# Optimization experiments

Hardware: AMD Instinct MI355X
Metric: run time of the kernel (lower is better)

Reference implementation:

```python
import jax, jax.numpy as jnp
import numpy as np

N = 50000   # nodes
E = 800000  # edges
F_IN, F_HID, F_OUT = 128, 96, 40


def setup_inputs() -> dict:
    key = jax.random.key(0)
    ks = jax.random.split(key, 9)
    x = jax.random.normal(ks[0], (N, F_IN), dtype=jnp.float32)
    edge_index = jax.random.randint(ks[1], (2, E), 0, N, dtype=jnp.int32)
    def lin(k, fi, fo):
        s = 1.0 / np.sqrt(fi)
        return jax.random.uniform(k, (fi, fo), jnp.float32, -s, s)
    W1 = lin(ks[2], F_IN, F_HID)
    b1 = jnp.zeros((F_HID,), jnp.float32)
    W2 = lin(ks[3], F_HID, F_HID)
    b2 = jnp.zeros((F_HID,), jnp.float32)
    Wout = lin(ks[4], F_HID, F_OUT)
    bout = jnp.zeros((F_OUT,), jnp.float32)
    return {"x": x, "edge_index": edge_index, "W1": W1, "b1": b1,
            "W2": W2, "b2": b2, "Wout": Wout, "bout": bout}


def _gcn_norm(edge_index, n):
    # add self-loops, symmetric degree normalization (PyG GCNConv default)
    loops = jnp.arange(n, dtype=edge_index.dtype)
    src = jnp.concatenate([edge_index[0], loops])
    dst = jnp.concatenate([edge_index[1], loops])
    deg = jax.ops.segment_sum(jnp.ones_like(dst, dtype=jnp.float32), dst,
                              num_segments=n)
    dinv = jnp.where(deg > 0, jax.lax.rsqrt(deg), 0.0)
    norm = dinv[src] * dinv[dst]   # [E+N]
    return src, dst, norm


def _gcn_layer(h, src, dst, norm, W, b, n):
    # linear transform, then normalized scatter-add aggregation, then bias
    h = h @ W                                 # [N, Fout]
    msg = h[src] * norm[:, None]              # gather + scale
    agg = jax.ops.segment_sum(msg, dst, num_segments=n)
    return agg + b


def reference(x, edge_index, W1, b1, W2, b2, Wout, bout):
    n = x.shape[0]
    src, dst, norm = _gcn_norm(edge_index, n)
    h = jax.nn.relu(_gcn_layer(x, src, dst, norm, W1, b1, n))
    h = jax.nn.relu(_gcn_layer(h, src, dst, norm, W2, b2, n))
    return h @ Wout + bout
```

## Files before the change

kernel.cpp:

```cpp
#include <hip/hip_runtime.h>
#include <hip/hip_fp16.h>

#define N_NODES 50000
#define N_EDGES 800000
#define F_INN   128
#define F_HID   96
#define F_OUTT  40
#define SLOTS   64

typedef _Float16 half8 __attribute__((ext_vector_type(8)));
typedef float    floatx4 __attribute__((ext_vector_type(4)));

template <int FI, typename TIN, bool SCALE>
__device__ __forceinline__ void mfma_gemm_body(
        const TIN* __restrict__ X, const __half* __restrict__ BTg,
        const float* __restrict__ dinv, float4* __restrict__ Th4, int n, int bx) {
    __shared__ __half BTl[96 * 136];
    __half* OUTl = BTl;
    int tid = threadIdx.x;
    {
        const int4* s = reinterpret_cast<const int4*>(BTg);
        int4* d = reinterpret_cast<int4*>(BTl);
        for (int i = tid; i < 96 * 136 / 8; i += 256) d[i] = s[i];
    }
    __syncthreads();

    int lane = tid & 63, w = tid >> 6;
    int lm = lane & 15, q = lane >> 4;
    int base = bx * 64 + w * 16;
    int node = base + lm;
    int nclamp = min(node, n - 1);
    const TIN* Xrow = X + (size_t)nclamp * FI;

    floatx4 cf[6];
    #pragma unroll
    for (int t = 0; t < 6; ++t) cf[t] = (floatx4){0.f, 0.f, 0.f, 0.f};

    constexpr int KS = FI / 32;
    #pragma unroll
    for (int ks = 0; ks < KS; ++ks) {
        half8 bv;
        if constexpr (sizeof(TIN) == 4) {
            const float4* xr = reinterpret_cast<const float4*>(Xrow + 32 * ks + q * 8);
            float4 f0 = xr[0], f1 = xr[1];
            union { half8 v; __half2 h[4]; } b;
            b.h[0] = __floats2half2_rn(f0.x, f0.y);
            b.h[1] = __floats2half2_rn(f0.z, f0.w);
            b.h[2] = __floats2half2_rn(f1.x, f1.y);
            b.h[3] = __floats2half2_rn(f1.z, f1.w);
            bv = b.v;
        } else {
            bv = *reinterpret_cast<const half8*>(Xrow + 32 * ks + q * 8);
        }
        #pragma unroll
        for (int t = 0; t < 6; ++t) {
            half8 a = *reinterpret_cast<const half8*>(
                &BTl[(t * 16 + lm) * 136 + q * 8 + 32 * ks]);
            cf[t] = __builtin_amdgcn_mfma_f32_16x16x32_f16(a, bv, cf[t], 0, 0, 0);
        }
    }

    float dv = 1.0f;
    if constexpr (SCALE) dv = dinv[nclamp];

    __syncthreads();

    __half* orow = OUTl + (w * 16 + lm) * 104;
    #pragma unroll
    for (int t = 0; t < 6; ++t) {
        union { int2 i2; __half2 h[2]; } u;
        u.h[0] = __floats2half2_rn(dv * cf[t][0], dv * cf[t][1]);
        u.h[1] = __floats2half2_rn(dv * cf[t][2], dv * cf[t][3]);
        *reinterpret_cast<int2*>(&orow[t * 16 + q * 4]) = u.i2;
    }
    #pragma unroll
    for (int R = 0; R < 3; ++R) {
        int nl = lane >> 2, c = (lane & 3) + 4 * R;
        float4 v = *reinterpret_cast<const float4*>(&OUTl[(w * 16 + nl) * 104 + c * 8]);
        int gn = base + nl;
        if (gn < n) Th4[(size_t)gn * 12 + c] = v;
    }
}

__global__ __launch_bounds__(256) void fill_gemm1_kernel(
        const int* __restrict__ src, const int* __restrict__ dst,
        int* __restrict__ cnt, int* __restrict__ csr_pad,
        int e, const float* __restrict__ X, const __half* __restrict__ BT1,
        float4* __restrict__ Th4, int n, int nFB) {
    if ((int)blockIdx.x < nFB) {
        int i = blockIdx.x * 512 + threadIdx.x;
        int j = i + 256;
        bool bi = i < e, bj = j < e;
        int di = 0, dj = 0, si, sj, pi, pj;
        if (bi) { di = dst[i]; si = src[i]; }
        if (bj) { dj = dst[j]; sj = src[j]; }
        if (bi) pi = atomicAdd(&cnt[di], 1);
        if (bj) pj = atomicAdd(&cnt[dj], 1);
        if (bi && pi < SLOTS) csr_pad[di * SLOTS + pi] = si;
        if (bj && pj < SLOTS) csr_pad[dj * SLOTS + pj] = sj;
    } else {
        mfma_gemm_body<F_INN, float, false>(X, BT1, nullptr, Th4, n, blockIdx.x - nFB);
    }
}

template <int FI, typename TIN, bool SCALE>
__global__ __launch_bounds__(256) void mfma_gemm_kernel(
        const TIN* __restrict__ X, const __half* __restrict__ BTg,
        const float* __restrict__ dinv, float4* __restrict__ Th4, int n) {
    mfma_gemm_body<FI, TIN, SCALE>(X, BTg, dinv, Th4, n, blockIdx.x);
}

__global__ void wt_kernel(const float* __restrict__ W1, const float* __restrict__ W2,
                          __half* __restrict__ BT1, __half* __restrict__ BT2) {
    int i = blockIdx.x * 256 + threadIdx.x;
    if (i < 96 * 128) {
        int j = i / 128, k = i - j * 128;
        BT1[j * 136 + k] = __float2half(W1[k * 96 + j]);
    } else if (i < 96 * 128 + 96 * 96) {
        int t = i - 96 * 128;
        int j = t / 96, k = t - j * 96;
        BT2[j * 136 + k] = __float2half(W2[k * 96 + j]);
    }
}

__global__ __launch_bounds__(256) void scale_dinv_kernel(
        const int* __restrict__ cnt, float* __restrict__ dinv,
        float4* __restrict__ Th4, int n) {
    int i = blockIdx.x * 256 + threadIdx.x;
    if (i < n) dinv[i] = rsqrtf((float)min(cnt[i], SLOTS) + 1.0f);
    if (i >= n * 12) return;
    int node = i / 12;
    float s = rsqrtf((float)min(cnt[node], SLOTS) + 1.0f);
    union { float4 f4; __half2 h[4]; } u;
    u.f4 = Th4[i];
    #pragma unroll
    for (int q = 0; q < 4; ++q) {
        float2 t = __half22float2(u.h[q]);
        u.h[q] = __floats2half2_rn(s * t.x, s * t.y);
    }
    Th4[i] = u.f4;
}

__global__ __launch_bounds__(256) void agg_kernel(
        const __half2* __restrict__ T, const int* __restrict__ cnt,
        const int* __restrict__ csr_pad, const float* __restrict__ dinv,
        const float* __restrict__ bias, __half2* __restrict__ H, int n) {
    int lane = threadIdx.x & 63;
    int node = __builtin_amdgcn_readfirstlane(blockIdx.x * 4 + (threadIdx.x >> 6));
    if (node >= n) return;
    int fl = min(lane, 47);

    float dn = dinv[node];
    float2 self = __half22float2(T[(size_t)node * 48 + fl]);
    float accx = self.x, accy = self.y;

    const int* row = csr_pad + (size_t)node * SLOTS;
    int deg = min(cnt[node], SLOTS);
    int idx = 0;
    for (; idx + 8 <= deg; idx += 8) {
        int s[8];
        #pragma unroll
        for (int u = 0; u < 8; ++u) s[u] = row[idx + u];
        float2 f[8];
        #pragma unroll
        for (int u = 0; u < 8; ++u) f[u] = __half22float2(T[(size_t)s[u] * 48 + fl]);
        #pragma unroll
        for (int u = 0; u < 8; ++u) {
            accx += f[u].x;
            accy += f[u].y;
        }
    }
    for (; idx < deg; ++idx) {
        int s = row[idx];
        float2 f = __half22float2(T[(size_t)s * 48 + fl]);
        accx += f.x;
        accy += f.y;
    }
    if (lane < 48) {
        float2 b = reinterpret_cast<const float2*>(bias)[lane];
        float ox = fmaxf(fmaf(dn, accx, b.x), 0.f);
        float oy = fmaxf(fmaf(dn, accy, b.y), 0.f);
        H[(size_t)node * 48 + lane] = __floats2half2_rn(ox, oy);
    }
}

__global__ __launch_bounds__(320) void gemm_out_kernel(
        const __half2* __restrict__ A, const float* __restrict__ W,
        const float* __restrict__ bias, float* __restrict__ C, int n) {
    __shared__ float Wlds[96 * 40];
    int tid = threadIdx.y * 10 + threadIdx.x;
    for (int i = tid; i < 96 * 10; i += 320)
        reinterpret_cast<float4*>(Wlds)[i] = reinterpret_cast<const float4*>(W)[i];
    __syncthreads();

    int j    = threadIdx.x * 4;
    int node = blockIdx.x * 32 + threadIdx.y;
    int nc   = min(node, n - 1);
    const __half2* Ah = A + (size_t)nc * 48;
    float4 acc = make_float4(0.f, 0.f, 0.f, 0.f);
    for (int k2 = 0; k2 < 48; k2 += 2) {
        float2 a01 = __half22float2(Ah[k2]);
        float2 a23 = __half22float2(Ah[k2 + 1]);
        int k = 2 * k2;
        float4 w0 = *reinterpret_cast<const float4*>(Wlds + (k + 0) * 40 + j);
        float4 w1 = *reinterpret_cast<const float4*>(Wlds + (k + 1) * 40 + j);
        float4 w2 = *reinterpret_cast<const float4*>(Wlds + (k + 2) * 40 + j);
        float4 w3 = *reinterpret_cast<const float4*>(Wlds + (k + 3) * 40 + j);
        acc.x += a01.x * w0.x + a01.y * w1.x + a23.x * w2.x + a23.y * w3.x;
        acc.y += a01.x * w0.y + a01.y * w1.y + a23.x * w2.y + a23.y * w3.y;
        acc.z += a01.x * w0.z + a01.y * w1.z + a23.x * w2.z + a23.y * w3.z;
        acc.w += a01.x * w0.w + a01.y * w1.w + a23.x * w2.w + a23.y * w3.w;
    }
    if (node < n) {
        float4 b = *reinterpret_cast<const float4*>(bias + j);
        acc.x += b.x; acc.y += b.y; acc.z += b.z; acc.w += b.w;
        *reinterpret_cast<float4*>(C + (size_t)node * 40 + j) = acc;
    }
}


extern "C" void kernel_launch(void* const* d_in, const int* in_sizes, int n_in,
                              void* d_out, int out_size, void* d_ws, size_t ws_size,
                              hipStream_t stream) {
    const float* x    = (const float*)d_in[0];
    const int*   ei   = (const int*)d_in[1];
    const float* W1   = (const float*)d_in[2];
    const float* b1   = (const float*)d_in[3];
    const float* W2   = (const float*)d_in[4];
    const float* b2   = (const float*)d_in[5];
    const float* Wout = (const float*)d_in[6];
    const float* bout = (const float*)d_in[7];
    float*       out  = (float*)d_out;

    const int* src = ei;
    const int* dst = ei + N_EDGES;

    char* ws = (char*)d_ws;
    size_t off = 0;
    auto alloc = [&](size_t bytes) {
        size_t o = off;
        off = (off + bytes + 511) & ~(size_t)511;
        return (void*)(ws + o);
    };
    int*     cnt       = (int*)    alloc((size_t)N_NODES * sizeof(int));
    float*   dinv      = (float*)  alloc(N_NODES * sizeof(float));
    int*     csr_pad   = (int*)    alloc((size_t)N_NODES * SLOTS * sizeof(int));
    __half*  BT1       = (__half*) alloc((size_t)96 * 136 * sizeof(__half));
    __half*  BT2       = (__half*) alloc((size_t)96 * 136 * sizeof(__half));
    __half2* Th        = (__half2*)alloc((size_t)N_NODES * 48 * sizeof(__half2));
    __half2* Hh        = (__half2*)alloc((size_t)N_NODES * 48 * sizeof(__half2));

    const int FB2 = (N_EDGES + 511) / 512;
    const int GB  = (N_NODES + 63) / 64;
    const int SB  = (N_NODES * 12 + 255) / 256;
    const int AB  = (N_NODES + 3) / 4;

    hipMemsetAsync(cnt, 0, (size_t)N_NODES * sizeof(int), stream);
    wt_kernel<<<(96 * 128 + 96 * 96 + 255) / 256, 256, 0, stream>>>(W1, W2, BT1, BT2);

    fill_gemm1_kernel<<<FB2 + GB, 256, 0, stream>>>(
        src, dst, cnt, csr_pad, N_EDGES, x, BT1, (float4*)Th, N_NODES, FB2);

    scale_dinv_kernel<<<SB, 256, 0, stream>>>(cnt, dinv, (float4*)Th, N_NODES);

    agg_kernel<<<AB, 256, 0, stream>>>(
        Th, cnt, csr_pad, dinv, b1, Hh, N_NODES);

    mfma_gemm_kernel<F_HID, __half, true><<<GB, 256, 0, stream>>>(
        (const __half*)Hh, BT2, dinv, (float4*)Th, N_NODES);
    agg_kernel<<<AB, 256, 0, stream>>>(
        Th, cnt, csr_pad, dinv, b2, Hh, N_NODES);

    gemm_out_kernel<<<(N_NODES + 31) / 32, dim3(10, 32), 0, stream>>>(
        Hh, Wout, bout, out, N_NODES);
}
```

Before: 225.1 us.

## Split CSR fill into count-with-rank pass and separate scatter pass

The edge pass alongside GEMM1 now only does the atomic degree count and records each edge's slot rank into a new rank array. The scattered csr_pad writes move into the following kernel, which also computes dinv and scales the transformed features. The aim is to shorten the atomic-heavy phase that overlaps the GEMM by taking the dependent scattered store out of it. In exchange it adds an 800K-int rank write and read plus a re-read of src and dst.

```diff
diff --git a/kernel.cpp b/kernel.cpp
--- a/kernel.cpp
+++ b/kernel.cpp
@@ -82,24 +82,23 @@
     }
 }
 
-__global__ __launch_bounds__(256) void fill_gemm1_kernel(
-        const int* __restrict__ src, const int* __restrict__ dst,
-        int* __restrict__ cnt, int* __restrict__ csr_pad,
+__global__ __launch_bounds__(256) void count_gemm1_kernel(
+        const int* __restrict__ dst, int* __restrict__ cnt, int* __restrict__ rank,
         int e, const float* __restrict__ X, const __half* __restrict__ BT1,
-        float4* __restrict__ Th4, int n, int nFB) {
-    if ((int)blockIdx.x < nFB) {
+        float4* __restrict__ Th4, int n, int nCB) {
+    if ((int)blockIdx.x < nCB) {
         int i = blockIdx.x * 512 + threadIdx.x;
         int j = i + 256;
         bool bi = i < e, bj = j < e;
-        int di = 0, dj = 0, si, sj, pi, pj;
-        if (bi) { di = dst[i]; si = src[i]; }
-        if (bj) { dj = dst[j]; sj = src[j]; }
-        if (bi) pi = atomicAdd(&cnt[di], 1);
-        if (bj) pj = atomicAdd(&cnt[dj], 1);
-        if (bi && pi < SLOTS) csr_pad[di * SLOTS + pi] = si;
-        if (bj && pj < SLOTS) csr_pad[dj * SLOTS + pj] = sj;
+        int di = 0, dj = 0, ri, rj;
+        if (bi) di = dst[i];
+        if (bj) dj = dst[j];
+        if (bi) ri = atomicAdd(&cnt[di], 1);
+        if (bj) rj = atomicAdd(&cnt[dj], 1);
+        if (bi) rank[i] = ri;
+        if (bj) rank[j] = rj;
     } else {
-        mfma_gemm_body<F_INN, float, false>(X, BT1, nullptr, Th4, n, blockIdx.x - nFB);
+        mfma_gemm_body<F_INN, float, false>(X, BT1, nullptr, Th4, n, blockIdx.x - nCB);
     }
 }
 
@@ -123,22 +122,31 @@
     }
 }
 
-__global__ __launch_bounds__(256) void scale_dinv_kernel(
+__global__ __launch_bounds__(256) void fill_scale_kernel(
+        const int* __restrict__ src, const int* __restrict__ dst,
+        const int* __restrict__ rank, int* __restrict__ csr_pad,
         const int* __restrict__ cnt, float* __restrict__ dinv,
-        float4* __restrict__ Th4, int n) {
-    int i = blockIdx.x * 256 + threadIdx.x;
-    if (i < n) dinv[i] = rsqrtf((float)min(cnt[i], SLOTS) + 1.0f);
-    if (i >= n * 12) return;
-    int node = i / 12;
-    float s = rsqrtf((float)min(cnt[node], SLOTS) + 1.0f);
-    union { float4 f4; __half2 h[4]; } u;
-    u.f4 = Th4[i];
-    #pragma unroll
-    for (int q = 0; q < 4; ++q) {
-        float2 t = __half22float2(u.h[q]);
-        u.h[q] = __floats2half2_rn(s * t.x, s * t.y);
-    }
-    Th4[i] = u.f4;
+        float4* __restrict__ Th4, int e, int n, int nFB) {
+    if ((int)blockIdx.x < nFB) {
+        int i = blockIdx.x * 256 + threadIdx.x;
+        if (i >= e) return;
+        int r = rank[i];
+        if (r < SLOTS) csr_pad[dst[i] * SLOTS + r] = src[i];
+    } else {
+        int i = (blockIdx.x - nFB) * 256 + threadIdx.x;
+        if (i < n) dinv[i] = rsqrtf((float)min(cnt[i], SLOTS) + 1.0f);
+        if (i >= n * 12) return;
+        int node = i / 12;
+        float s = rsqrtf((float)min(cnt[node], SLOTS) + 1.0f);
+        union { float4 f4; __half2 h[4]; } u;
+        u.f4 = Th4[i];
+        #pragma unroll
+        for (int q = 0; q < 4; ++q) {
+            float2 t = __half22float2(u.h[q]);
+            u.h[q] = __floats2half2_rn(s * t.x, s * t.y);
+        }
+        Th4[i] = u.f4;
+    }
 }
 
 __global__ __launch_bounds__(256) void agg_kernel(
@@ -244,24 +252,27 @@
     };
     int*     cnt       = (int*)    alloc((size_t)N_NODES * sizeof(int));
     float*   dinv      = (float*)  alloc(N_NODES * sizeof(float));
+    int*     rank      = (int*)    alloc((size_t)N_EDGES * sizeof(int));
     int*     csr_pad   = (int*)    alloc((size_t)N_NODES * SLOTS * sizeof(int));
     __half*  BT1       = (__half*) alloc((size_t)96 * 136 * sizeof(__half));
     __half*  BT2       = (__half*) alloc((size_t)96 * 136 * sizeof(__half));
     __half2* Th        = (__half2*)alloc((size_t)N_NODES * 48 * sizeof(__half2));
     __half2* Hh        = (__half2*)alloc((size_t)N_NODES * 48 * sizeof(__half2));
 
-    const int FB2 = (N_EDGES + 511) / 512;
+    const int CB2 = (N_EDGES + 511) / 512;
+    const int FB  = (N_EDGES + 255) / 256;
+    const int SB  = (N_NODES * 12 + 255) / 256;
     const int GB  = (N_NODES + 63) / 64;
-    const int SB  = (N_NODES * 12 + 255) / 256;
     const int AB  = (N_NODES + 3) / 4;
 
     hipMemsetAsync(cnt, 0, (size_t)N_NODES * sizeof(int), stream);
     wt_kernel<<<(96 * 128 + 96 * 96 + 255) / 256, 256, 0, stream>>>(W1, W2, BT1, BT2);
 
-    fill_gemm1_kernel<<<FB2 + GB, 256, 0, stream>>>(
-        src, dst, cnt, csr_pad, N_EDGES, x, BT1, (float4*)Th, N_NODES, FB2);
-
-    scale_dinv_kernel<<<SB, 256, 0, stream>>>(cnt, dinv, (float4*)Th, N_NODES);
+    count_gemm1_kernel<<<CB2 + GB, 256, 0, stream>>>(
+        dst, cnt, rank, N_EDGES, x, BT1, (float4*)Th, N_NODES, CB2);
+
+    fill_scale_kernel<<<FB + SB, 256, 0, stream>>>(
+        src, dst, rank, csr_pad, cnt, dinv, (float4*)Th, N_EDGES, N_NODES, FB);
 
     agg_kernel<<<AB, 256, 0, stream>>>(
         Th, cnt, csr_pad, dinv, b1, Hh, N_NODES);
```

Measured after the change: 223.7 us (median of 2 runs). No clear change (-0.6%).
